# Optimization experiments

Measured on AMD Instinct MI355X. Metric: run time of the kernel, lower is better.

The kernel has to match this reference:

```python
import jax, jax.numpy as jnp
import numpy as np

N, E, B = 100000, 3200000, 64      # nodes, edges, graphs
F_IN, E_IN, A = 64, 16, 13          # node feat, edge feat, action dim
H, OUT = 32, 64                     # GENConv hidden / out channels
EPS_GEN, EPS_BN = 1e-7, 1e-5


def setup_inputs() -> dict:
    key = jax.random.key(0)
    ks = jax.random.split(key, 32)

    def w(k, shape):
        scale = 1.0 / np.sqrt(shape[0])
        return jax.random.uniform(k, shape, jnp.float32, -scale, scale)

    inp = {}
    inp["x"] = jax.random.normal(ks[0], (N, F_IN), jnp.float32)
    inp["edge_index"] = jax.random.randint(ks[1], (2, E), 0, N)
    inp["edge_attr"] = jax.random.normal(ks[2], (E, E_IN), jnp.float32)
    inp["batch"] = jnp.sort(jax.random.randint(ks[3], (N,), 0, B))
    inp["action"] = jax.random.normal(ks[4], (B, A), jnp.float32)
    # encoders
    inp["node_w"] = w(ks[5], (F_IN, H)); inp["node_b"] = jnp.zeros((H,), jnp.float32)
    inp["edge_w"] = w(ks[6], (E_IN, H)); inp["edge_b"] = jnp.zeros((H,), jnp.float32)
    # GENConv internal MLP: channels [32,64,64,64,64], BN+ReLU between hidden layers
    inp["mlp_w1"] = w(ks[7], (H, OUT));   inp["mlp_b1"] = jnp.zeros((OUT,), jnp.float32)
    inp["bn1_g"] = jnp.ones((OUT,), jnp.float32); inp["bn1_b"] = jnp.zeros((OUT,), jnp.float32)
    inp["mlp_w2"] = w(ks[8], (OUT, OUT)); inp["mlp_b2"] = jnp.zeros((OUT,), jnp.float32)
    inp["bn2_g"] = jnp.ones((OUT,), jnp.float32); inp["bn2_b"] = jnp.zeros((OUT,), jnp.float32)
    inp["mlp_w3"] = w(ks[9], (OUT, OUT)); inp["mlp_b3"] = jnp.zeros((OUT,), jnp.float32)
    inp["bn3_g"] = jnp.ones((OUT,), jnp.float32); inp["bn3_b"] = jnp.zeros((OUT,), jnp.float32)
    inp["mlp_w4"] = w(ks[10], (OUT, OUT)); inp["mlp_b4"] = jnp.zeros((OUT,), jnp.float32)
    # policy head
    inp["pin_w"] = w(ks[11], (OUT, 16));  inp["pin_b"] = jnp.zeros((16,), jnp.float32)
    inp["ph_w"] = w(ks[12], (16 + A, 10)); inp["ph_b"] = jnp.zeros((10,), jnp.float32)
    inp["po_w"] = jax.random.uniform(ks[13], (10, 1), jnp.float32, -0.003, 0.003)
    inp["po_b"] = jnp.zeros((1,), jnp.float32)
    return inp


def _bn(h, g, b):
    # BatchNorm1d, training-mode batch statistics (biased variance)
    mu = h.mean(axis=0)
    var = h.var(axis=0)
    return g * (h - mu) * jax.lax.rsqrt(var + EPS_BN) + b


def reference(x, edge_index, edge_attr, batch, action,
              node_w, node_b, edge_w, edge_b,
              mlp_w1, mlp_b1, bn1_g, bn1_b,
              mlp_w2, mlp_b2, bn2_g, bn2_b,
              mlp_w3, mlp_b3, bn3_g, bn3_b,
              mlp_w4, mlp_b4,
              pin_w, pin_b, ph_w, ph_b, po_w, po_b):
    h = x @ node_w + node_b                      # [N, 32]
    ea = edge_attr @ edge_w + edge_b             # [E, 32]
    src, dst = edge_index[0], edge_index[1]
    # GENConv message: relu(x_j + e) + eps
    msg = jax.nn.relu(h[src] + ea) + EPS_GEN     # [E, 32]
    # softmax aggregation over destination neighborhoods (t = 1.0)
    mx = jax.ops.segment_max(msg, dst, num_segments=N)   # [N, 32]
    ex = jnp.exp(msg - mx[dst])
    sm = jax.ops.segment_sum(ex, dst, num_segments=N)
    alpha = ex / sm[dst]
    agg = jax.ops.segment_sum(msg * alpha, dst, num_segments=N)
    out = agg + h                                # add root
    # internal MLP: Lin-BN-ReLU x3, then Lin
    h1 = jax.nn.relu(_bn(out @ mlp_w1 + mlp_b1, bn1_g, bn1_b))
    h2 = jax.nn.relu(_bn(h1 @ mlp_w2 + mlp_b2, bn2_g, bn2_b))
    h3 = jax.nn.relu(_bn(h2 @ mlp_w3 + mlp_b3, bn3_g, bn3_b))
    node_out = h3 @ mlp_w4 + mlp_b4              # [N, 64]
    # global mean pool per graph
    sums = jax.ops.segment_sum(node_out, batch, num_segments=B)
    cnt = jax.ops.segment_sum(jnp.ones((node_out.shape[0], 1), node_out.dtype), batch, num_segments=B)
    mol = sums / jnp.maximum(cnt, 1.0)           # [B, 64]
    fp = jax.nn.relu(mol @ pin_w + pin_b)        # [B, 16]
    pol = jax.nn.relu(jnp.concatenate([fp, action], axis=1) @ ph_w + ph_b)
    return pol @ po_w + po_b                     # [B, 1]
```

## Files before the change

### kernel.cpp

```cpp
#include <hip/hip_runtime.h>
#include <cstdint>
#include <cstddef>


#define N_NODES 100000
#define N_EDGES 3200000
#define B_GRAPHS 64
#define F_INF 64
#define E_INF 16
#define A_DIM 13
#define H_DIM 32
#define O_DIM 64
#define EPS_GEN 1e-7f
#define EPS_BN 1e-5f
#define SCAN_BLOCKS 391

__global__ __launch_bounds__(256) void k_node_enc(
        const float* __restrict__ x, const float* __restrict__ w,
        const float* __restrict__ b, float* __restrict__ h) {
    __shared__ float sW[F_INF * H_DIM];
    __shared__ float sB[H_DIM];
    __shared__ float sX[8 * F_INF];
    int tid = threadIdx.x;
    for (int i = tid; i < F_INF * H_DIM; i += 256) sW[i] = w[i];
    if (tid < H_DIM) sB[tid] = b[tid];
    int node0 = blockIdx.x * 8;
    const float2* xp = (const float2*)(x + (size_t)node0 * F_INF);
    float2 v = xp[tid];
    sX[2 * tid] = v.x;
    sX[2 * tid + 1] = v.y;
    __syncthreads();
    int nl = tid >> 5, ch = tid & 31;
    float acc = sB[ch];
    const float* xr = &sX[nl * F_INF];
#pragma unroll
    for (int k = 0; k < F_INF; k++) acc = fmaf(xr[k], sW[k * H_DIM + ch], acc);
    h[(size_t)(node0 + nl) * H_DIM + ch] = acc;
}

__global__ __launch_bounds__(256) void k_hist(
        const int* __restrict__ ei, int* __restrict__ deg) {
    int i = blockIdx.x * 256 + threadIdx.x;
    if (i >= N_EDGES / 4) return;
    int4 d = ((const int4*)(ei + N_EDGES))[i];
    atomicAdd(&deg[d.x], 1);
    atomicAdd(&deg[d.y], 1);
    atomicAdd(&deg[d.z], 1);
    atomicAdd(&deg[d.w], 1);
}

__global__ __launch_bounds__(256) void k_scan1(
        const int* __restrict__ deg, int* __restrict__ incl,
        int* __restrict__ bsum) {
    __shared__ int s[256];
    int tid = threadIdx.x;
    int i = blockIdx.x * 256 + tid;
    int v = (i < N_NODES) ? deg[i] : 0;
    s[tid] = v;
    __syncthreads();
    for (int d = 1; d < 256; d <<= 1) {
        int t = (tid >= d) ? s[tid - d] : 0;
        __syncthreads();
        s[tid] += t;
        __syncthreads();
    }
    if (i < N_NODES) incl[i] = s[tid];
    if (tid == 255) bsum[blockIdx.x] = s[255];
}

__global__ __launch_bounds__(512) void k_scan2(int* __restrict__ bsum) {
    __shared__ int s[512];
    int t = threadIdx.x;
    int v = (t < SCAN_BLOCKS) ? bsum[t] : 0;
    s[t] = v;
    __syncthreads();
    for (int d = 1; d < 512; d <<= 1) {
        int tv = (t >= d) ? s[t - d] : 0;
        __syncthreads();
        s[t] += tv;
        __syncthreads();
    }
    if (t < SCAN_BLOCKS) bsum[t] = s[t] - v;
}

__global__ __launch_bounds__(256) void k_scan3(
        int* __restrict__ deg_offs, int* __restrict__ incl_cursor,
        const int* __restrict__ bsum) {
    int i = blockIdx.x * 256 + threadIdx.x;
    if (i >= N_NODES) return;
    int o = bsum[i >> 8] + incl_cursor[i] - deg_offs[i];
    deg_offs[i] = o;
    incl_cursor[i] = o;
    if (i == 0) deg_offs[N_NODES] = N_EDGES;
}

__global__ __launch_bounds__(256) void k_scatter_perm(
        const int* __restrict__ ei, int* __restrict__ cursor,
        const float* __restrict__ ea, float* __restrict__ eap,
        int* __restrict__ srcp) {
    int e = blockIdx.x * 256 + threadIdx.x;
    if (e >= N_EDGES) return;
    int src = ei[e];
    int d = ei[N_EDGES + e];
    const float4* er = (const float4*)(ea + (size_t)e * E_INF);
    float4 q0 = er[0], q1 = er[1], q2 = er[2], q3 = er[3];
    int pos = atomicAdd(&cursor[d], 1);
    float4* wr = (float4*)(eap + (size_t)pos * E_INF);
    wr[0] = q0; wr[1] = q1; wr[2] = q2; wr[3] = q3;
    srcp[pos] = src;
}

__global__ __launch_bounds__(256) void k_scatter_idx(
        const int* __restrict__ ei, int* __restrict__ cursor,
        uint2* __restrict__ sorted) {
    int e = blockIdx.x * 256 + threadIdx.x;
    if (e >= N_EDGES) return;
    int src = ei[e];
    int d = ei[N_EDGES + e];
    int pos = atomicAdd(&cursor[d], 1);
    sorted[pos] = make_uint2((unsigned)e, (unsigned)src);
}

template <bool PERM>
__global__ __launch_bounds__(256, 4) void k_gather(
        const float* __restrict__ easrc, const int* __restrict__ srcp,
        const uint2* __restrict__ sorted, const int* __restrict__ offs,
        const float* __restrict__ ew, const float* __restrict__ eb,
        const float* __restrict__ h, float* __restrict__ conv) {
    __shared__ float sEA[4 * 2 * 256];
    int tid = threadIdx.x;
    int wave = tid >> 6, lane = tid & 63;
    int p = lane >> 5;
    int j = lane & 31;
    int v = blockIdx.x * 4 + wave;
    int s0 = offs[v], s1 = offs[v + 1];
    float wj[16];
#pragma unroll
    for (int k = 0; k < 16; k++) wj[k] = ew[k * H_DIM + j];
    float bj = eb[j];
    float hv = h[(size_t)v * H_DIM + j];
    float se = 0.0f, sme = 0.0f;
    float* myEA = &sEA[wave * 512];

    if (s0 < s1) {
        const int s1m1 = s1 - 1;
        const int w16 = lane & 15;
        const int row4 = lane >> 2;
        const int part = lane & 3;
        float hs_cur[8], hs_next[8];
        float4 st;
        uint2 srtN = make_uint2(0u, 0u);
        unsigned scN = 0;
        int c = s0, buf = 0;
        {
            unsigned sc0;
            if constexpr (PERM) {
                sc0 = (unsigned)srcp[min(c + w16, s1m1)];
                st = ((const float4*)easrc)[(size_t)min(c + row4, s1m1) * 4 + part];
            } else {
                uint2 srt0 = sorted[min(c + w16, s1m1)];
                sc0 = srt0.y;
                unsigned eid = (unsigned)__shfl((int)srt0.x, row4);
                st = ((const float4*)easrc)[(size_t)eid * 4 + part];
            }
#pragma unroll
            for (int t = 0; t < 8; t++) {
                int sc = __shfl((int)sc0, 2 * t + p);
                hs_cur[t] = h[(size_t)sc * H_DIM + j];
            }
            if constexpr (PERM) scN = (unsigned)srcp[min(c + 16 + w16, s1m1)];
            else srtN = sorted[min(c + 16 + w16, s1m1)];
            ((float4*)myEA)[lane] = st;
        }
        for (;;) {
            bool more = (c + 16 < s1);
            if (more) {
                if constexpr (PERM) {
                    st = ((const float4*)easrc)[(size_t)min(c + 16 + row4, s1m1) * 4 + part];
                } else {
                    unsigned eid = (unsigned)__shfl((int)srtN.x, row4);
                    st = ((const float4*)easrc)[(size_t)eid * 4 + part];
                }
                unsigned scsrc = PERM ? scN : srtN.y;
#pragma unroll
                for (int t = 0; t < 8; t++) {
                    int sc = __shfl((int)scsrc, 2 * t + p);
                    hs_next[t] = h[(size_t)sc * H_DIM + j];
                }
                if constexpr (PERM) scN = (unsigned)srcp[min(c + 32 + w16, s1m1)];
                else srtN = sorted[min(c + 32 + w16, s1m1)];
            }
            const float* cb = &myEA[buf * 256];
#pragma unroll
            for (int t = 0; t < 8; t++) {
                int e = 2 * t + p;
                if (c + e < s1) {
                    const float4* er = (const float4*)&cb[e * 16];
                    float4 q0 = er[0], q1 = er[1], q2 = er[2], q3 = er[3];
                    float acc = bj;
                    acc = fmaf(q0.x, wj[0], acc);
                    acc = fmaf(q0.y, wj[1], acc);
                    acc = fmaf(q0.z, wj[2], acc);
                    acc = fmaf(q0.w, wj[3], acc);
                    acc = fmaf(q1.x, wj[4], acc);
                    acc = fmaf(q1.y, wj[5], acc);
                    acc = fmaf(q1.z, wj[6], acc);
                    acc = fmaf(q1.w, wj[7], acc);
                    acc = fmaf(q2.x, wj[8], acc);
                    acc = fmaf(q2.y, wj[9], acc);
                    acc = fmaf(q2.z, wj[10], acc);
                    acc = fmaf(q2.w, wj[11], acc);
                    acc = fmaf(q3.x, wj[12], acc);
                    acc = fmaf(q3.y, wj[13], acc);
                    acc = fmaf(q3.z, wj[14], acc);
                    acc = fmaf(q3.w, wj[15], acc);
                    float m = fmaxf(acc + hs_cur[t], 0.0f) + EPS_GEN;
                    float ex = __expf(m);
                    se += ex;
                    sme += m * ex;
                }
            }
            if (!more) break;
            ((float4*)(myEA + (buf ^ 1) * 256))[lane] = st;
#pragma unroll
            for (int t = 0; t < 8; t++) hs_cur[t] = hs_next[t];
            c += 16;
            buf ^= 1;
        }
    }
    se += __shfl_xor(se, 32);
    sme += __shfl_xor(sme, 32);
    if (p == 0) {
        float r = (se > 0.0f) ? (sme / se) : 0.0f;
        conv[(size_t)v * H_DIM + j] = r + hv;
    }
}

template <int IN_CH, bool BN_IN, bool STATS>
__global__ __launch_bounds__(256) void k_lin(
        const float* __restrict__ in, const float* __restrict__ w,
        const float* __restrict__ b, const float* __restrict__ ss,
        float* __restrict__ out, float* __restrict__ stats) {
    __shared__ float sW[IN_CH * O_DIM];
    __shared__ float sB[O_DIM];
    __shared__ float sS[IN_CH], sH[IN_CH];
    __shared__ float sX[16 * IN_CH];
    __shared__ float r1[256], r2[256];
    int tid = threadIdx.x;
    for (int i = tid; i < IN_CH * O_DIM; i += 256) sW[i] = w[i];
    if (tid < O_DIM) sB[tid] = b[tid];
    if constexpr (BN_IN) {
        if (tid < IN_CH) { sS[tid] = ss[tid]; sH[tid] = ss[64 + tid]; }
    }
    int ch = tid & 63, nl = tid >> 6;
    float s1 = 0.0f, s2 = 0.0f;
    const int ngroups = N_NODES / 16;
    __syncthreads();
    for (int g = blockIdx.x; g < ngroups; g += gridDim.x) {
        size_t base = (size_t)g * 16 * IN_CH;
        __syncthreads();
        if constexpr (IN_CH == 64) {
            float4 v = ((const float4*)(in + base))[tid];
            if constexpr (BN_IN) {
                int c0 = (tid * 4) & 63;
                v.x = fmaxf(fmaf(v.x, sS[c0], sH[c0]), 0.0f);
                v.y = fmaxf(fmaf(v.y, sS[c0 + 1], sH[c0 + 1]), 0.0f);
                v.z = fmaxf(fmaf(v.z, sS[c0 + 2], sH[c0 + 2]), 0.0f);
                v.w = fmaxf(fmaf(v.w, sS[c0 + 3], sH[c0 + 3]), 0.0f);
            }
            ((float4*)sX)[tid] = v;
        } else {
            float2 v = ((const float2*)(in + base))[tid];
            if constexpr (BN_IN) {
                int c0 = (tid * 2) & (IN_CH - 1);
                v.x = fmaxf(fmaf(v.x, sS[c0], sH[c0]), 0.0f);
                v.y = fmaxf(fmaf(v.y, sS[c0 + 1], sH[c0 + 1]), 0.0f);
            }
            ((float2*)sX)[tid] = v;
        }
        __syncthreads();
#pragma unroll
        for (int q = 0; q < 4; q++) {
            const float* xr = &sX[(nl + 4 * q) * IN_CH];
            float acc = sB[ch];
#pragma unroll
            for (int k = 0; k < IN_CH; k++) acc = fmaf(xr[k], sW[k * O_DIM + ch], acc);
            out[(size_t)(g * 16 + nl + 4 * q) * O_DIM + ch] = acc;
            if constexpr (STATS) { s1 += acc; s2 += acc * acc; }
        }
    }
    if constexpr (STATS) {
        __syncthreads();
        r1[tid] = s1; r2[tid] = s2;
        __syncthreads();
        if (tid < 64) {
            float a1 = r1[tid] + r1[tid + 64] + r1[tid + 128] + r1[tid + 192];
            float a2 = r2[tid] + r2[tid + 64] + r2[tid + 128] + r2[tid + 192];
            unsafeAtomicAdd(&stats[tid], a1);
            unsafeAtomicAdd(&stats[64 + tid], a2);
        }
    }
}

__global__ void k_bnfin(const float* __restrict__ stats, const float* __restrict__ g,
                        const float* __restrict__ b, float* __restrict__ ss) {
    int c = threadIdx.x;
    if (c >= 64) return;
    const float invN = 1.0f / (float)N_NODES;
    float mu = stats[c] * invN;
    float var = fmaxf(stats[64 + c] * invN - mu * mu, 0.0f);
    float rs = 1.0f / sqrtf(var + EPS_BN);
    float sc = g[c] * rs;
    ss[c] = sc;
    ss[64 + c] = b[c] - mu * sc;
}

__global__ void k_bounds(const int* __restrict__ batch, int* __restrict__ start) {
    int g = threadIdx.x;
    if (g > B_GRAPHS) return;
    int lo = 0, hi = N_NODES;
    while (lo < hi) {
        int mid = (lo + hi) >> 1;
        if (batch[mid] < g) lo = mid + 1; else hi = mid;
    }
    start[g] = lo;
}

__global__ __launch_bounds__(256) void k_pool(
        const float* __restrict__ no, const int* __restrict__ start,
        float* __restrict__ gsum) {
    int g = blockIdx.x >> 2, q = blockIdx.x & 3;
    int s0 = start[g], s1e = start[g + 1];
    int len = s1e - s0;
    int per = (len + 3) >> 2;
    int a = s0 + q * per;
    int bnd = min(s0 + (q + 1) * per, s1e);
    int ch = threadIdx.x & 63, nl = threadIdx.x >> 6;
    float acc = 0.0f;
    for (int n = a + nl; n < bnd; n += 4) acc += no[(size_t)n * O_DIM + ch];
    __shared__ float r[256];
    r[threadIdx.x] = acc;
    __syncthreads();
    if (threadIdx.x < 64) {
        float v = r[ch] + r[ch + 64] + r[ch + 128] + r[ch + 192];
        unsafeAtomicAdd(&gsum[g * O_DIM + ch], v);
    }
}

__global__ void k_head(const float* __restrict__ gsum, const int* __restrict__ start,
                       const float* __restrict__ action,
                       const float* __restrict__ pinw, const float* __restrict__ pinb,
                       const float* __restrict__ phw, const float* __restrict__ phb,
                       const float* __restrict__ pow_, const float* __restrict__ pob,
                       float* __restrict__ outp) {
    int g = threadIdx.x;
    if (g >= B_GRAPHS) return;
    int cnt = start[g + 1] - start[g];
    float inv = 1.0f / (float)max(cnt, 1);
    float mol[64];
#pragma unroll
    for (int c = 0; c < 64; c++) mol[c] = gsum[g * 64 + c] * inv;
    float fp[16];
#pragma unroll
    for (int j = 0; j < 16; j++) {
        float a = pinb[j];
        for (int c = 0; c < 64; c++) a = fmaf(mol[c], pinw[c * 16 + j], a);
        fp[j] = fmaxf(a, 0.0f);
    }
    float pol[10];
#pragma unroll
    for (int j = 0; j < 10; j++) {
        float a = phb[j];
        for (int k = 0; k < 16; k++) a = fmaf(fp[k], phw[k * 10 + j], a);
        for (int k = 0; k < 13; k++) a = fmaf(action[g * 13 + k], phw[(16 + k) * 10 + j], a);
        pol[j] = fmaxf(a, 0.0f);
    }
    float o = pob[0];
#pragma unroll
    for (int j = 0; j < 10; j++) o = fmaf(pol[j], pow_[j], o);
    outp[g] = o;
}

extern "C" void kernel_launch(void* const* d_in, const int* in_sizes, int n_in,
                              void* d_out, int out_size, void* d_ws, size_t ws_size,
                              hipStream_t stream) {
    const float* x      = (const float*)d_in[0];
    const int*   ei     = (const int*)d_in[1];
    const float* ea     = (const float*)d_in[2];
    const int*   batch  = (const int*)d_in[3];
    const float* action = (const float*)d_in[4];
    const float* node_w = (const float*)d_in[5];
    const float* node_b = (const float*)d_in[6];
    const float* edge_w = (const float*)d_in[7];
    const float* edge_b = (const float*)d_in[8];
    const float* w1 = (const float*)d_in[9];   const float* b1 = (const float*)d_in[10];
    const float* g1 = (const float*)d_in[11];  const float* bb1 = (const float*)d_in[12];
    const float* w2 = (const float*)d_in[13];  const float* b2 = (const float*)d_in[14];
    const float* g2 = (const float*)d_in[15];  const float* bb2 = (const float*)d_in[16];
    const float* w3 = (const float*)d_in[17];  const float* b3 = (const float*)d_in[18];
    const float* g3 = (const float*)d_in[19];  const float* bb3 = (const float*)d_in[20];
    const float* w4 = (const float*)d_in[21];  const float* b4 = (const float*)d_in[22];
    const float* pinw = (const float*)d_in[23]; const float* pinb = (const float*)d_in[24];
    const float* phw  = (const float*)d_in[25]; const float* phb  = (const float*)d_in[26];
    const float* pow_ = (const float*)d_in[27]; const float* pob  = (const float*)d_in[28];

    char* wsb = (char*)d_ws;
    size_t off = 0;
    float* stats  = (float*)(wsb + off); off += 512 * 4;
    float* gsum   = (float*)(wsb + off); off += 4096 * 4;
    int*   offs   = (int*)  (wsb + off); off += 400128;
    size_t zero_bytes = off;
    int*   cursor = (int*)  (wsb + off); off += 400128;
    int*   bsum   = (int*)  (wsb + off); off += 2048;
    float* ssb    = (float*)(wsb + off); off += 512 * 4;
    int*   start  = (int*)  (wsb + off); off += 512;
    int*   srcp   = (int*)  (wsb + off); off += (size_t)N_EDGES * 4;
    float* h      = (float*)(wsb + off); off += (size_t)N_NODES * H_DIM * 4;
    float* conv   = (float*)(wsb + off); off += (size_t)N_NODES * H_DIM * 4;
    size_t tail = off;
    bool perm = (ws_size >= tail + (size_t)N_EDGES * E_INF * 4);
    float* eap    = (float*)(wsb + tail);
    uint2* sorted = (uint2*)(wsb + tail);
    float* t1, *t2;
    if (perm) {
        t1 = eap;
        t2 = eap + (size_t)N_NODES * O_DIM;
    } else {
        t1 = (float*)sorted;
        t2 = h;
    }

    hipMemsetAsync(d_ws, 0, zero_bytes, stream);

    k_node_enc<<<N_NODES / 8, 256, 0, stream>>>(x, node_w, node_b, h);
    k_hist<<<(N_EDGES / 4 + 255) / 256, 256, 0, stream>>>(ei, offs);
    k_scan1<<<SCAN_BLOCKS, 256, 0, stream>>>(offs, cursor, bsum);
    k_scan2<<<1, 512, 0, stream>>>(bsum);
    k_scan3<<<SCAN_BLOCKS, 256, 0, stream>>>(offs, cursor, bsum);
    if (perm) {
        k_scatter_perm<<<(N_EDGES + 255) / 256, 256, 0, stream>>>(ei, cursor, ea, eap, srcp);
        k_gather<true><<<N_NODES / 4, 256, 0, stream>>>(eap, srcp, nullptr, offs,
                                                        edge_w, edge_b, h, conv);
    } else {
        k_scatter_idx<<<(N_EDGES + 255) / 256, 256, 0, stream>>>(ei, cursor, sorted);
        k_gather<false><<<N_NODES / 4, 256, 0, stream>>>(ea, nullptr, sorted, offs,
                                                         edge_w, edge_b, h, conv);
    }
    k_lin<32, false, true><<<1250, 256, 0, stream>>>(conv, w1, b1, nullptr, t1, stats + 0);
    k_bnfin<<<1, 64, 0, stream>>>(stats + 0, g1, bb1, ssb + 0);
    k_lin<64, true, true><<<1250, 256, 0, stream>>>(t1, w2, b2, ssb + 0, t2, stats + 128);
    k_bnfin<<<1, 64, 0, stream>>>(stats + 128, g2, bb2, ssb + 128);
    k_lin<64, true, true><<<1250, 256, 0, stream>>>(t2, w3, b3, ssb + 128, t1, stats + 256);
    k_bnfin<<<1, 64, 0, stream>>>(stats + 256, g3, bb3, ssb + 256);
    k_lin<64, true, false><<<1250, 256, 0, stream>>>(t1, w4, b4, ssb + 256, t2, nullptr);
    k_bounds<<<1, 128, 0, stream>>>(batch, start);
    k_pool<<<B_GRAPHS * 4, 256, 0, stream>>>(t2, start, gsum);
    k_head<<<1, 64, 0, stream>>>(gsum, start, action, pinw, pinb, phw, phb, pow_, pob,
                                 (float*)d_out);
}
```

Before: 1.020 ms.

## Drop permuted edge-feature copy and scatter edge indices four per thread

Removes the path that physically permuted the 16-float edge attributes into destination order, and always writes only (edge id, src) pairs and gathers edge attributes indirectly in the aggregation kernel. This avoids writing and rereading a full permuted copy of the edge-feature array. In exchange, the gather reads edge features non-contiguously. The index scatter kernel now loads src/dst as int4 and handles four edges per thread to cut the thread count and widen the loads.

```diff
diff --git a/kernel.cpp b/kernel.cpp
--- a/kernel.cpp
+++ b/kernel.cpp
@@ -94,31 +94,22 @@
     if (i == 0) deg_offs[N_NODES] = N_EDGES;
 }
 
-__global__ __launch_bounds__(256) void k_scatter_perm(
-        const int* __restrict__ ei, int* __restrict__ cursor,
-        const float* __restrict__ ea, float* __restrict__ eap,
-        int* __restrict__ srcp) {
-    int e = blockIdx.x * 256 + threadIdx.x;
-    if (e >= N_EDGES) return;
-    int src = ei[e];
-    int d = ei[N_EDGES + e];
-    const float4* er = (const float4*)(ea + (size_t)e * E_INF);
-    float4 q0 = er[0], q1 = er[1], q2 = er[2], q3 = er[3];
-    int pos = atomicAdd(&cursor[d], 1);
-    float4* wr = (float4*)(eap + (size_t)pos * E_INF);
-    wr[0] = q0; wr[1] = q1; wr[2] = q2; wr[3] = q3;
-    srcp[pos] = src;
-}
-
 __global__ __launch_bounds__(256) void k_scatter_idx(
         const int* __restrict__ ei, int* __restrict__ cursor,
         uint2* __restrict__ sorted) {
-    int e = blockIdx.x * 256 + threadIdx.x;
-    if (e >= N_EDGES) return;
-    int src = ei[e];
-    int d = ei[N_EDGES + e];
-    int pos = atomicAdd(&cursor[d], 1);
-    sorted[pos] = make_uint2((unsigned)e, (unsigned)src);
+    int i = blockIdx.x * 256 + threadIdx.x;
+    if (i >= N_EDGES / 4) return;
+    int4 s = ((const int4*)ei)[i];
+    int4 d = ((const int4*)(ei + N_EDGES))[i];
+    int e0 = i * 4;
+    int p0 = atomicAdd(&cursor[d.x], 1);
+    sorted[p0] = make_uint2((unsigned)(e0 + 0), (unsigned)s.x);
+    int p1 = atomicAdd(&cursor[d.y], 1);
+    sorted[p1] = make_uint2((unsigned)(e0 + 1), (unsigned)s.y);
+    int p2 = atomicAdd(&cursor[d.z], 1);
+    sorted[p2] = make_uint2((unsigned)(e0 + 2), (unsigned)s.z);
+    int p3 = atomicAdd(&cursor[d.w], 1);
+    sorted[p3] = make_uint2((unsigned)(e0 + 3), (unsigned)s.w);
 }
 
 template <bool PERM>
@@ -418,17 +409,10 @@
     float* h      = (float*)(wsb + off); off += (size_t)N_NODES * H_DIM * 4;
     float* conv   = (float*)(wsb + off); off += (size_t)N_NODES * H_DIM * 4;
     size_t tail = off;
-    bool perm = (ws_size >= tail + (size_t)N_EDGES * E_INF * 4);
-    float* eap    = (float*)(wsb + tail);
+    (void)srcp;
     uint2* sorted = (uint2*)(wsb + tail);
-    float* t1, *t2;
-    if (perm) {
-        t1 = eap;
-        t2 = eap + (size_t)N_NODES * O_DIM;
-    } else {
-        t1 = (float*)sorted;
-        t2 = h;
-    }
+    float* t1 = (float*)sorted;
+    float* t2 = h;
 
     hipMemsetAsync(d_ws, 0, zero_bytes, stream);
 
@@ -437,15 +421,9 @@
     k_scan1<<<SCAN_BLOCKS, 256, 0, stream>>>(offs, cursor, bsum);
     k_scan2<<<1, 512, 0, stream>>>(bsum);
     k_scan3<<<SCAN_BLOCKS, 256, 0, stream>>>(offs, cursor, bsum);
-    if (perm) {
-        k_scatter_perm<<<(N_EDGES + 255) / 256, 256, 0, stream>>>(ei, cursor, ea, eap, srcp);
-        k_gather<true><<<N_NODES / 4, 256, 0, stream>>>(eap, srcp, nullptr, offs,
-                                                        edge_w, edge_b, h, conv);
-    } else {
-        k_scatter_idx<<<(N_EDGES + 255) / 256, 256, 0, stream>>>(ei, cursor, sorted);
-        k_gather<false><<<N_NODES / 4, 256, 0, stream>>>(ea, nullptr, sorted, offs,
-                                                         edge_w, edge_b, h, conv);
-    }
+    k_scatter_idx<<<(N_EDGES / 4 + 255) / 256, 256, 0, stream>>>(ei, cursor, sorted);
+    k_gather<false><<<N_NODES / 4, 256, 0, stream>>>(ea, nullptr, sorted, offs,
+                                                     edge_w, edge_b, h, conv);
     k_lin<32, false, true><<<1250, 256, 0, stream>>>(conv, w1, b1, nullptr, t1, stats + 0);
     k_bnfin<<<1, 64, 0, stream>>>(stats + 0, g1, bb1, ssb + 0);
     k_lin<64, true, true><<<1250, 256, 0, stream>>>(t1, w2, b2, ssb + 0, t2, stats + 128);
```

Measured after the change: 1.102 ms. 1.08x slower.
